# Kernel optimization log

Hardware: AMD Instinct MI355X
Metric: run time of the kernel (lower is better)

## Reference

```python
import jax, jax.numpy as jnp
import numpy as np

N_QUBITS = 8   # out_channels = number of wires
KERNEL = 4     # kernel_size
N_LAYERS = 4
STRIDE = 1
PAD = 1


def _rx(t):
    c = jnp.cos(t * 0.5).astype(jnp.complex64)
    s = jnp.sin(t * 0.5).astype(jnp.complex64)
    return jnp.stack([jnp.stack([c, -1j * s]), jnp.stack([-1j * s, c])])


def _ry(t):
    c = jnp.cos(t * 0.5).astype(jnp.complex64)
    s = jnp.sin(t * 0.5).astype(jnp.complex64)
    return jnp.stack([jnp.stack([c, -s]), jnp.stack([s, c])])


def _rz(t):
    e = jnp.exp(-0.5j * t.astype(jnp.complex64))
    z = jnp.zeros((), jnp.complex64)
    return jnp.stack([jnp.stack([e, z]), jnp.stack([z, jnp.conj(e)])])


def _ap1(state, U, w):
    # apply 2x2 gate U on qubit axis w of state shaped (2,)*N_QUBITS
    s = jnp.moveaxis(state, w, -1)
    s = s @ U.T
    return jnp.moveaxis(s, -1, w)


def _cnot(state, c, t):
    s0 = jax.lax.index_in_dim(state, 0, axis=c, keepdims=True)
    s1 = jax.lax.index_in_dim(state, 1, axis=c, keepdims=True)
    return jnp.concatenate([s0, jnp.flip(s1, axis=t)], axis=c)


def _ansatz(state, wl):  # wl: (N_QUBITS, 3) angles for layer i (custom_layers)
    for j in range(N_QUBITS):
        c, t = (j, j + 1) if j < N_QUBITS - 1 else (0, j)
        state = _ap1(state, _rx(wl[j, 0]), j)
        state = _cnot(state, c, t)
        state = _ap1(state, _ry(wl[j, 1]), j)
        state = _cnot(state, c, t)
        state = _ap1(state, _rz(wl[j, 2]), j)
    return state


def _circuit(inputs, weights):
    # inputs: (KERNEL,) patch; weights: (N_LAYERS+1, N_QUBITS, 3)
    state = jnp.zeros((2,) * N_QUBITS, jnp.complex64).at[(0,) * N_QUBITS].set(1.0)
    state = _ansatz(state, weights[0])
    for i in range(1, N_LAYERS + 1):
        w = 0
        for _ in range(N_QUBITS // KERNEL):  # 'parallel': re-upload data each layer
            for k in range(KERNEL):
                state = _ap1(state, _ry(inputs[k]), w + k)
            w += KERNEL
        state = _ansatz(state, weights[i])
    probs = state.real ** 2 + state.imag ** 2
    sign = jnp.array([1.0, -1.0], jnp.float32)
    z = [jnp.sum(probs, axis=tuple(a for a in range(N_QUBITS) if a != j)) @ sign
         for j in range(N_QUBITS)]
    return jnp.stack(z)  # (N_QUBITS,) <PauliZ_j>


def _forward(vector, weights):
    bs, ch, l = vector.shape
    if ch > 1:
        vector = vector.mean(axis=-2).reshape(bs, 1, l)
    v = jnp.pad(vector, ((0, 0), (0, 0), (PAD, PAD)))
    l_out = (l + 2 * PAD - KERNEL) // STRIDE + 1
    idx = jnp.arange(l_out)[:, None] * STRIDE + jnp.arange(KERNEL)  # (l_out, K)
    patches = v[:, 0, :][:, idx].reshape(bs * l_out, KERNEL)
    q = jax.vmap(_circuit, in_axes=(0, None))(patches, weights)  # (bs*l_out, N_QUBITS)
    out = q.reshape(bs, l_out, N_QUBITS).transpose(0, 2, 1)  # (bs, C, l_out)
    out = jax.nn.relu(out)
    return jnp.max(out, axis=-1, keepdims=True)  # (bs, C, 1)


def setup_inputs() -> dict:
    key = jax.random.key(0)
    k1, k2 = jax.random.split(key)
    vector = jax.random.normal(k1, (8, 1, 512), jnp.float32)
    # flax nn.initializers.normal() default stddev = 0.01
    weights = jax.random.normal(k2, (N_LAYERS + 1, N_QUBITS, 3), jnp.float32) * 0.01
    return {"vector": vector, "weights": weights}


def reference(vector, weights):
    return _forward(vector, weights)
```

## Files before the change

### kernel.cpp

```cpp
#include <hip/hip_runtime.h>

#define NQ 8
#define KK 4
#define LIN 512
#define LOUT 511
#define BATCH 8
#define NCIRC (BATCH * LOUT)

__device__ float g_tab[240];
__device__ float g_st0[512];

template<int M> __device__ __forceinline__ float lx(float v) {
    if constexpr (M == 1)
        return __builtin_bit_cast(float, __builtin_amdgcn_update_dpp(
            0, __builtin_bit_cast(int, v), 0xB1, 0xF, 0xF, true));
    else if constexpr (M == 2)
        return __builtin_bit_cast(float, __builtin_amdgcn_update_dpp(
            0, __builtin_bit_cast(int, v), 0x4E, 0xF, 0xF, true));
    else if constexpr (M == 3)
        return __builtin_bit_cast(float, __builtin_amdgcn_update_dpp(
            0, __builtin_bit_cast(int, v), 0x1B, 0xF, 0xF, true));
    else if constexpr (M == 8)
        return __builtin_bit_cast(float, __builtin_amdgcn_update_dpp(
            0, __builtin_bit_cast(int, v), 0x128, 0xF, 0xF, true));
    else if constexpr (M < 32)
        return __builtin_bit_cast(float, __builtin_amdgcn_ds_swizzle(
            __builtin_bit_cast(int, v), (M << 10) | 0x1F));
    else
        return __shfl_xor(v, M, 64);
}

template<int BP>
__device__ __forceinline__ void g_rx4(float (&sr)[4], float (&si)[4], float c, float s, int lane) {
    if constexpr (BP >= 2) {
        constexpr int M = 1 << (BP - 2);
        #pragma unroll
        for (int r = 0; r < 4; ++r) {
            float orr = lx<M>(sr[r]), oii = lx<M>(si[r]);
            float nr = c * sr[r] + s * oii;
            float ni = c * si[r] - s * orr;
            sr[r] = nr; si[r] = ni;
        }
    } else if constexpr (BP == 1) {
        #pragma unroll
        for (int p = 0; p < 2; ++p) {
            const int a = p, b = p + 2;
            float ar = sr[a], ai = si[a], br = sr[b], bi = si[b];
            sr[a] = c*ar + s*bi;  si[a] = c*ai - s*br;
            sr[b] = c*br + s*ai;  si[b] = c*bi - s*ar;
        }
    } else {
        #pragma unroll
        for (int p = 0; p < 2; ++p) {
            const int a = 2*p, b = 2*p + 1;
            float ar = sr[a], ai = si[a], br = sr[b], bi = si[b];
            sr[a] = c*ar + s*bi;  si[a] = c*ai - s*br;
            sr[b] = c*br + s*ai;  si[b] = c*bi - s*ar;
        }
    }
}

template<int BP>
__device__ __forceinline__ void g_rz4(float (&sr)[4], float (&si)[4], float c, float s, int lane) {
    if constexpr (BP >= 2) {
        const float t = ((lane >> (BP - 2)) & 1) ? -s : s;
        #pragma unroll
        for (int r = 0; r < 4; ++r) {
            float nr = c * sr[r] + t * si[r];
            float ni = c * si[r] - t * sr[r];
            sr[r] = nr; si[r] = ni;
        }
    } else if constexpr (BP == 1) {
        #pragma unroll
        for (int r = 0; r < 4; ++r) {
            const float t = (r < 2) ? s : -s;
            float nr = c * sr[r] + t * si[r];
            float ni = c * si[r] - t * sr[r];
            sr[r] = nr; si[r] = ni;
        }
    } else {
        #pragma unroll
        for (int r = 0; r < 4; ++r) {
            const float t = ((r & 1) == 0) ? s : -s;
            float nr = c * sr[r] + t * si[r];
            float ni = c * si[r] - t * sr[r];
            sr[r] = nr; si[r] = ni;
        }
    }
}

template<int BPC, int BPT>
__device__ __forceinline__ void g_fry4(float (&sr)[4], float (&si)[4], float c, float s, int lane) {
    if constexpr (BPT >= 2) {
        constexpr int M = (1 << (BPC - 2)) | (1 << (BPT - 2));
        const float sg = ((lane >> (BPC - 2)) & 1) ? s : -s;
        #pragma unroll
        for (int r = 0; r < 4; ++r) {
            float orr = lx<M>(sr[r]), oii = lx<M>(si[r]);
            sr[r] = c * sr[r] + sg * orr;
            si[r] = c * si[r] + sg * oii;
        }
    } else if constexpr (BPT == 1) {
        constexpr int M = 1 << (BPC - 2);
        const float sg = ((lane >> (BPC - 2)) & 1) ? s : -s;
        float pr[4], pi[4];
        #pragma unroll
        for (int r = 0; r < 4; ++r) { pr[r] = lx<M>(sr[r ^ 2]); pi[r] = lx<M>(si[r ^ 2]); }
        #pragma unroll
        for (int r = 0; r < 4; ++r) { sr[r] = c*sr[r] + sg*pr[r]; si[r] = c*si[r] + sg*pi[r]; }
    } else if constexpr (BPC == 1) {
        float t0r = sr[0], t0i = si[0], t1r = sr[1], t1i = si[1];
        sr[0] = c*sr[0] - s*sr[3];  si[0] = c*si[0] - s*si[3];
        sr[1] = c*sr[1] - s*sr[2];  si[1] = c*si[1] - s*si[2];
        sr[2] = c*sr[2] + s*t1r;    si[2] = c*si[2] + s*t1i;
        sr[3] = c*sr[3] + s*t0r;    si[3] = c*si[3] + s*t0i;
    } else {
        constexpr int M = 1 << (BPC - 2);
        const float sg = ((lane >> (BPC - 2)) & 1) ? s : -s;
        float pr[4], pi[4];
        #pragma unroll
        for (int r = 0; r < 4; ++r) { pr[r] = lx<M>(sr[r ^ 1]); pi[r] = lx<M>(si[r ^ 1]); }
        #pragma unroll
        for (int r = 0; r < 4; ++r) { sr[r] = c*sr[r] + sg*pr[r]; si[r] = c*si[r] + sg*pi[r]; }
    }
}

__device__ __forceinline__ void g_cry4_q7(float (&sr)[4], float (&si)[4], float c, float s, int lane) {
    const float se = ((lane >> 5) & 1) ? -s : s;
    #pragma unroll
    for (int p = 0; p < 2; ++p) {
        const int a = 2*p, b = 2*p + 1;
        float ar = sr[a], ai = si[a], br = sr[b], bi = si[b];
        sr[a] = c*ar - se*br;  si[a] = c*ai - se*bi;
        sr[b] = se*ar + c*br;  si[b] = se*ai + c*bi;
    }
}

template<int J>
__device__ __forceinline__ void astep4(float (&sr)[4], float (&si)[4],
                                       const float* __restrict__ t48, int lane) {
    constexpr int BP = 7 - J;
    g_rx4<BP>(sr, si, t48[J*6 + 0], t48[J*6 + 1], lane);
    if constexpr (J < 7) {
        g_fry4<7 - J, 6 - J>(sr, si, t48[J*6 + 2], t48[J*6 + 3], lane);
    } else {
        g_cry4_q7(sr, si, t48[J*6 + 2], t48[J*6 + 3], lane);
    }
    g_rz4<BP>(sr, si, t48[J*6 + 4], t48[J*6 + 5], lane);
}

template<int LB>
__device__ __forceinline__ void rx_lane(float (&sr)[8], float (&si)[8], float c, float s) {
    constexpr int M = 1 << LB;
    #pragma unroll
    for (int r = 0; r < 8; ++r) {
        float orr = lx<M>(sr[r]), oii = lx<M>(si[r]);
        float nr = c * sr[r] + s * oii;
        float ni = c * si[r] - s * orr;
        sr[r] = nr; si[r] = ni;
    }
}

template<int LB>
__device__ __forceinline__ void ry_lane(float (&sr)[8], float (&si)[8], float c, float s, int lane) {
    constexpr int M = 1 << LB;
    const float sg = ((lane >> LB) & 1) ? s : -s;
    #pragma unroll
    for (int r = 0; r < 8; ++r) {
        float orr = lx<M>(sr[r]), oii = lx<M>(si[r]);
        sr[r] = c * sr[r] + sg * orr;
        si[r] = c * si[r] + sg * oii;
    }
}

template<int LB>
__device__ __forceinline__ void rz_lane(float (&sr)[8], float (&si)[8], float c, float s, int lane) {
    const float t = ((lane >> LB) & 1) ? -s : s;
    #pragma unroll
    for (int r = 0; r < 8; ++r) {
        float nr = c * sr[r] + t * si[r];
        float ni = c * si[r] - t * sr[r];
        sr[r] = nr; si[r] = ni;
    }
}

template<int RB>
__device__ __forceinline__ void rx_reg(float (&sr)[8], float (&si)[8], float c, float s) {
    constexpr int m = 1 << RB;
    #pragma unroll
    for (int r = 0; r < 8; ++r) {
        if ((r & m) == 0) {
            const int a = r, b = r | m;
            float ar = sr[a], ai = si[a], br = sr[b], bi = si[b];
            sr[a] = c*ar + s*bi;  si[a] = c*ai - s*br;
            sr[b] = c*br + s*ai;  si[b] = c*bi - s*ar;
        }
    }
}

template<int RB>
__device__ __forceinline__ void ry_reg(float (&sr)[8], float (&si)[8], float c, float s) {
    constexpr int m = 1 << RB;
    #pragma unroll
    for (int r = 0; r < 8; ++r) {
        if ((r & m) == 0) {
            const int a = r, b = r | m;
            float ar = sr[a], ai = si[a], br = sr[b], bi = si[b];
            sr[a] = c*ar - s*br;  si[a] = c*ai - s*bi;
            sr[b] = s*ar + c*br;  si[b] = s*ai + c*bi;
        }
    }
}

template<int RB>
__device__ __forceinline__ void rz_reg(float (&sr)[8], float (&si)[8], float c, float s) {
    #pragma unroll
    for (int r = 0; r < 8; ++r) {
        const float t = ((r >> RB) & 1) ? -s : s;
        float nr = c * sr[r] + t * si[r];
        float ni = c * si[r] - t * sr[r];
        sr[r] = nr; si[r] = ni;
    }
}

template<int LBc, int LBt>
__device__ __forceinline__ void fry_ll(float (&sr)[8], float (&si)[8], float c, float s, int lane) {
    constexpr int M = (1 << LBc) | (1 << LBt);
    const float sg = ((lane >> LBc) & 1) ? s : -s;
    #pragma unroll
    for (int r = 0; r < 8; ++r) {
        float orr = lx<M>(sr[r]), oii = lx<M>(si[r]);
        sr[r] = c * sr[r] + sg * orr;
        si[r] = c * si[r] + sg * oii;
    }
}

template<int LBc, int RBt>
__device__ __forceinline__ void fry_lr(float (&sr)[8], float (&si)[8], float c, float s, int lane) {
    constexpr int M = 1 << LBc;
    constexpr int mt = 1 << RBt;
    const float sg = ((lane >> LBc) & 1) ? s : -s;
    float pr[8], pi[8];
    #pragma unroll
    for (int r = 0; r < 8; ++r) { pr[r] = lx<M>(sr[r ^ mt]); pi[r] = lx<M>(si[r ^ mt]); }
    #pragma unroll
    for (int r = 0; r < 8; ++r) { sr[r] = c*sr[r] + sg*pr[r]; si[r] = c*si[r] + sg*pi[r]; }
}

template<int RBc, int RBt>
__device__ __forceinline__ void fry_rr(float (&sr)[8], float (&si)[8], float c, float s) {
    constexpr int mm = (1 << RBc) | (1 << RBt);
    float nr[8], ni[8];
    #pragma unroll
    for (int r = 0; r < 8; ++r) {
        const float sg = ((r >> RBc) & 1) ? s : -s;
        nr[r] = c*sr[r] + sg*sr[r ^ mm];
        ni[r] = c*si[r] + sg*si[r ^ mm];
    }
    #pragma unroll
    for (int r = 0; r < 8; ++r) { sr[r] = nr[r]; si[r] = ni[r]; }
}

__device__ __forceinline__ void cry_q7(float (&sr)[8], float (&si)[8], float c, float s, int lane) {
    const float se = ((lane >> 4) & 1) ? -s : s;
    #pragma unroll
    for (int p = 0; p < 4; ++p) {
        const int a = 2*p, b = 2*p + 1;
        float ar = sr[a], ai = si[a], br = sr[b], bi = si[b];
        sr[a] = c*ar - se*br;  si[a] = c*ai - se*bi;
        sr[b] = se*ar + c*br;  si[b] = se*ai + c*bi;
    }
}

template<bool LAST>
__device__ __forceinline__ void ansatz8(float (&sr)[8], float (&si)[8],
                                        const float* __restrict__ t, int lane) {
    rx_lane<4>(sr, si, t[0], t[1]);
    fry_ll<4,3>(sr, si, t[2], t[3], lane);
    if (!LAST) rz_lane<4>(sr, si, t[4], t[5], lane);
    rx_lane<3>(sr, si, t[6], t[7]);
    fry_ll<3,2>(sr, si, t[8], t[9], lane);
    if (!LAST) rz_lane<3>(sr, si, t[10], t[11], lane);
    rx_lane<2>(sr, si, t[12], t[13]);
    fry_ll<2,1>(sr, si, t[14], t[15], lane);
    if (!LAST) rz_lane<2>(sr, si, t[16], t[17], lane);
    rx_lane<1>(sr, si, t[18], t[19]);
    fry_ll<1,0>(sr, si, t[20], t[21], lane);
    if (!LAST) rz_lane<1>(sr, si, t[22], t[23], lane);
    rx_lane<0>(sr, si, t[24], t[25]);
    fry_lr<0,2>(sr, si, t[26], t[27], lane);
    if (!LAST) rz_lane<0>(sr, si, t[28], t[29], lane);
    rx_reg<2>(sr, si, t[30], t[31]);
    fry_rr<2,1>(sr, si, t[32], t[33]);
    if (!LAST) rz_reg<2>(sr, si, t[34], t[35]);
    rx_reg<1>(sr, si, t[36], t[37]);
    fry_rr<1,0>(sr, si, t[38], t[39]);
    if (!LAST) rz_reg<1>(sr, si, t[40], t[41]);
    rx_reg<0>(sr, si, t[42], t[43]);
    cry_q7(sr, si, t[44], t[45], lane);
    if (!LAST) rz_reg<0>(sr, si, t[46], t[47]);
}

__device__ __forceinline__ void reup8(float (&sr)[8], float (&si)[8],
                                      const float (&xc)[4], const float (&xs)[4], int lane) {
    ry_lane<4>(sr, si, xc[0], xs[0], lane);  ry_lane<0>(sr, si, xc[0], xs[0], lane);
    ry_lane<3>(sr, si, xc[1], xs[1], lane);  ry_reg<2>(sr, si, xc[1], xs[1]);
    ry_lane<2>(sr, si, xc[2], xs[2], lane);  ry_reg<1>(sr, si, xc[2], xs[2]);
    ry_lane<1>(sr, si, xc[3], xs[3], lane);  ry_reg<0>(sr, si, xc[3], xs[3]);
}

template<int ST>
__device__ __forceinline__ void bstage8(float (&z)[8], int lane) {
    constexpr int M = 1 << ST;
    #pragma unroll
    for (int q = 0; q < 8; ++q) {
        float o = lx<M>(z[q]);
        if (q < 5 && (4 - q) == ST)
            z[q] = ((lane >> ST) & 1) ? (o - z[q]) : (z[q] - o);
        else
            z[q] += o;
    }
}

__global__ __launch_bounds__(256) void prep_kernel(const float* __restrict__ wts,
                                                   float* __restrict__ out) {
    __shared__ float tt[240];
    const int t = threadIdx.x;
    if (t < 120) {
        float a = 0.5f * wts[t];
        float cv = __cosf(a), sv = __sinf(a);
        g_tab[2*t] = cv;  g_tab[2*t + 1] = sv;
        tt[2*t] = cv;     tt[2*t + 1] = sv;
    }
    if (t >= 192 && t < 192 + BATCH * NQ) out[t - 192] = 0.0f;
    __syncthreads();
    if (t < 64) {
        const int lane = t;
        float sr[4] = {0.f, 0.f, 0.f, 0.f};
        float si[4] = {0.f, 0.f, 0.f, 0.f};
        if (lane == 0) sr[0] = 1.0f;
        astep4<0>(sr, si, tt, lane); astep4<1>(sr, si, tt, lane);
        astep4<2>(sr, si, tt, lane); astep4<3>(sr, si, tt, lane);
        astep4<4>(sr, si, tt, lane); astep4<5>(sr, si, tt, lane);
        astep4<6>(sr, si, tt, lane); astep4<7>(sr, si, tt, lane);
        #pragma unroll
        for (int r = 0; r < 4; ++r) {
            g_st0[(lane*4 + r)*2]     = sr[r];
            g_st0[(lane*4 + r)*2 + 1] = si[r];
        }
    }
}

__global__ __launch_bounds__(256) void quanv_kernel(const float* __restrict__ vec,
                                                    float* __restrict__ out) {
    const int tid = threadIdx.x;
    const int lane = tid & 63;
    const int pos = tid & 31;
    const int circ = blockIdx.x * 8 + (tid >> 5);
    const int b = circ / LOUT;
    const int op = circ - b * LOUT;

    float xc[4], xs[4];
    #pragma unroll
    for (int k = 0; k < KK; ++k) {
        int idx = op - 1 + k;
        int ic = idx < 0 ? 0 : (idx > LIN - 1 ? LIN - 1 : idx);
        float xv = vec[b * LIN + ic];
        xv = (idx == ic) ? xv : 0.0f;
        float a = 0.5f * xv;
        xs[k] = __sinf(a); xc[k] = __cosf(a);
    }

    float sr[8], si[8];
    {
        const float4* st4 = (const float4*)g_st0;
        #pragma unroll
        for (int h = 0; h < 4; ++h) {
            float4 v4 = st4[pos * 4 + h];
            sr[2*h]   = v4.x; si[2*h]   = v4.y;
            sr[2*h+1] = v4.z; si[2*h+1] = v4.w;
        }
    }

    #pragma unroll 1
    for (int L = 1; L <= 3; ++L) {
        reup8(sr, si, xc, xs, lane);
        ansatz8<false>(sr, si, g_tab + L * 48, lane);
    }
    reup8(sr, si, xc, xs, lane);
    ansatz8<true>(sr, si, g_tab + 4 * 48, lane);

    float p[8];
    #pragma unroll
    for (int r = 0; r < 8; ++r) p[r] = sr[r]*sr[r] + si[r]*si[r];
    float pl = 0.f, z5 = 0.f, z6 = 0.f, z7 = 0.f;
    #pragma unroll
    for (int r = 0; r < 8; ++r) {
        pl += p[r];
        z5 += ((r >> 2) & 1) ? -p[r] : p[r];
        z6 += ((r >> 1) & 1) ? -p[r] : p[r];
        z7 += ( r       & 1) ? -p[r] : p[r];
    }
    float z[8];
    z[0] = pl; z[1] = pl; z[2] = pl; z[3] = pl; z[4] = pl;
    z[5] = z5; z[6] = z6; z[7] = z7;

    bstage8<0>(z, lane); bstage8<1>(z, lane); bstage8<2>(z, lane);
    bstage8<3>(z, lane); bstage8<4>(z, lane);

    __shared__ float zsh[8][NQ];
    __shared__ int bsh[8];
    const int g = tid >> 5;
    if (pos == 0) {
        bsh[g] = b;
        #pragma unroll
        for (int q = 0; q < NQ; ++q) zsh[g][q] = fmaxf(z[q], 0.0f);
    }
    __syncthreads();
    if (tid < 64) {
        const int gg = tid >> 3, q = tid & 7;
        const bool leader = (gg == 0) || (bsh[gg] != bsh[gg - 1]);
        if (leader) {
            float m = zsh[gg][q];
            for (int g2 = gg + 1; g2 < 8 && bsh[g2] == bsh[gg]; ++g2)
                m = fmaxf(m, zsh[g2][q]);
            atomicMax((unsigned int*)(out + bsh[gg] * NQ + q), __float_as_uint(m));
        }
    }
}

extern "C" void kernel_launch(void* const* d_in, const int* in_sizes, int n_in,
                              void* d_out, int out_size, void* d_ws, size_t ws_size,
                              hipStream_t stream) {
    const float* vec = (const float*)d_in[0];
    const float* wts = (const float*)d_in[1];
    float* out = (float*)d_out;

    hipLaunchKernelGGL(prep_kernel, dim3(1), dim3(256), 0, stream, wts, out);
    const int blocks = NCIRC / 8;
    hipLaunchKernelGGL(quanv_kernel, dim3(blocks), dim3(256), 0, stream, vec, out);
}
```

Measured before the change: 75.45 us.

## Fuse prep kernel into main kernel with in-kernel trig and last-block finalize

```diff
diff --git a/kernel.cpp b/kernel.cpp
--- a/kernel.cpp
+++ b/kernel.cpp
@@ -6,9 +6,11 @@
 #define LOUT 511
 #define BATCH 8
 #define NCIRC (BATCH * LOUT)
-
-__device__ float g_tab[240];
-__device__ float g_st0[512];
+#define NBLOCKS (NCIRC / 8)
+
+#define ENC0 0xC0000000u
+__device__ unsigned g_acc[BATCH * NQ];
+__device__ unsigned g_cnt;
 
 template<int M> __device__ __forceinline__ float lx(float v) {
     if constexpr (M == 1)
@@ -23,130 +25,9 @@
     else if constexpr (M == 8)
         return __builtin_bit_cast(float, __builtin_amdgcn_update_dpp(
             0, __builtin_bit_cast(int, v), 0x128, 0xF, 0xF, true));
-    else if constexpr (M < 32)
+    else
         return __builtin_bit_cast(float, __builtin_amdgcn_ds_swizzle(
             __builtin_bit_cast(int, v), (M << 10) | 0x1F));
-    else
-        return __shfl_xor(v, M, 64);
-}
-
-template<int BP>
-__device__ __forceinline__ void g_rx4(float (&sr)[4], float (&si)[4], float c, float s, int lane) {
-    if constexpr (BP >= 2) {
-        constexpr int M = 1 << (BP - 2);
-        #pragma unroll
-        for (int r = 0; r < 4; ++r) {
-            float orr = lx<M>(sr[r]), oii = lx<M>(si[r]);
-            float nr = c * sr[r] + s * oii;
-            float ni = c * si[r] - s * orr;
-            sr[r] = nr; si[r] = ni;
-        }
-    } else if constexpr (BP == 1) {
-        #pragma unroll
-        for (int p = 0; p < 2; ++p) {
-            const int a = p, b = p + 2;
-            float ar = sr[a], ai = si[a], br = sr[b], bi = si[b];
-            sr[a] = c*ar + s*bi;  si[a] = c*ai - s*br;
-            sr[b] = c*br + s*ai;  si[b] = c*bi - s*ar;
-        }
-    } else {
-        #pragma unroll
-        for (int p = 0; p < 2; ++p) {
-            const int a = 2*p, b = 2*p + 1;
-            float ar = sr[a], ai = si[a], br = sr[b], bi = si[b];
-            sr[a] = c*ar + s*bi;  si[a] = c*ai - s*br;
-            sr[b] = c*br + s*ai;  si[b] = c*bi - s*ar;
-        }
-    }
-}
-
-template<int BP>
-__device__ __forceinline__ void g_rz4(float (&sr)[4], float (&si)[4], float c, float s, int lane) {
-    if constexpr (BP >= 2) {
-        const float t = ((lane >> (BP - 2)) & 1) ? -s : s;
-        #pragma unroll
-        for (int r = 0; r < 4; ++r) {
-            float nr = c * sr[r] + t * si[r];
-            float ni = c * si[r] - t * sr[r];
-            sr[r] = nr; si[r] = ni;
-        }
-    } else if constexpr (BP == 1) {
-        #pragma unroll
-        for (int r = 0; r < 4; ++r) {
-            const float t = (r < 2) ? s : -s;
-            float nr = c * sr[r] + t * si[r];
-            float ni = c * si[r] - t * sr[r];
-            sr[r] = nr; si[r] = ni;
-        }
-    } else {
-        #pragma unroll
-        for (int r = 0; r < 4; ++r) {
-            const float t = ((r & 1) == 0) ? s : -s;
-            float nr = c * sr[r] + t * si[r];
-            float ni = c * si[r] - t * sr[r];
-            sr[r] = nr; si[r] = ni;
-        }
-    }
-}
-
-template<int BPC, int BPT>
-__device__ __forceinline__ void g_fry4(float (&sr)[4], float (&si)[4], float c, float s, int lane) {
-    if constexpr (BPT >= 2) {
-        constexpr int M = (1 << (BPC - 2)) | (1 << (BPT - 2));
-        const float sg = ((lane >> (BPC - 2)) & 1) ? s : -s;
-        #pragma unroll
-        for (int r = 0; r < 4; ++r) {
-            float orr = lx<M>(sr[r]), oii = lx<M>(si[r]);
-            sr[r] = c * sr[r] + sg * orr;
-            si[r] = c * si[r] + sg * oii;
-        }
-    } else if constexpr (BPT == 1) {
-        constexpr int M = 1 << (BPC - 2);
-        const float sg = ((lane >> (BPC - 2)) & 1) ? s : -s;
-        float pr[4], pi[4];
-        #pragma unroll
-        for (int r = 0; r < 4; ++r) { pr[r] = lx<M>(sr[r ^ 2]); pi[r] = lx<M>(si[r ^ 2]); }
-        #pragma unroll
-        for (int r = 0; r < 4; ++r) { sr[r] = c*sr[r] + sg*pr[r]; si[r] = c*si[r] + sg*pi[r]; }
-    } else if constexpr (BPC == 1) {
-        float t0r = sr[0], t0i = si[0], t1r = sr[1], t1i = si[1];
-        sr[0] = c*sr[0] - s*sr[3];  si[0] = c*si[0] - s*si[3];
-        sr[1] = c*sr[1] - s*sr[2];  si[1] = c*si[1] - s*si[2];
-        sr[2] = c*sr[2] + s*t1r;    si[2] = c*si[2] + s*t1i;
-        sr[3] = c*sr[3] + s*t0r;    si[3] = c*si[3] + s*t0i;
-    } else {
-        constexpr int M = 1 << (BPC - 2);
-        const float sg = ((lane >> (BPC - 2)) & 1) ? s : -s;
-        float pr[4], pi[4];
-        #pragma unroll
-        for (int r = 0; r < 4; ++r) { pr[r] = lx<M>(sr[r ^ 1]); pi[r] = lx<M>(si[r ^ 1]); }
-        #pragma unroll
-        for (int r = 0; r < 4; ++r) { sr[r] = c*sr[r] + sg*pr[r]; si[r] = c*si[r] + sg*pi[r]; }
-    }
-}
-
-__device__ __forceinline__ void g_cry4_q7(float (&sr)[4], float (&si)[4], float c, float s, int lane) {
-    const float se = ((lane >> 5) & 1) ? -s : s;
-    #pragma unroll
-    for (int p = 0; p < 2; ++p) {
-        const int a = 2*p, b = 2*p + 1;
-        float ar = sr[a], ai = si[a], br = sr[b], bi = si[b];
-        sr[a] = c*ar - se*br;  si[a] = c*ai - se*bi;
-        sr[b] = se*ar + c*br;  si[b] = se*ai + c*bi;
-    }
-}
-
-template<int J>
-__device__ __forceinline__ void astep4(float (&sr)[4], float (&si)[4],
-                                       const float* __restrict__ t48, int lane) {
-    constexpr int BP = 7 - J;
-    g_rx4<BP>(sr, si, t48[J*6 + 0], t48[J*6 + 1], lane);
-    if constexpr (J < 7) {
-        g_fry4<7 - J, 6 - J>(sr, si, t48[J*6 + 2], t48[J*6 + 3], lane);
-    } else {
-        g_cry4_q7(sr, si, t48[J*6 + 2], t48[J*6 + 3], lane);
-    }
-    g_rz4<BP>(sr, si, t48[J*6 + 4], t48[J*6 + 5], lane);
 }
 
 template<int LB>
@@ -274,31 +155,31 @@
 
 template<bool LAST>
 __device__ __forceinline__ void ansatz8(float (&sr)[8], float (&si)[8],
-                                        const float* __restrict__ t, int lane) {
-    rx_lane<4>(sr, si, t[0], t[1]);
-    fry_ll<4,3>(sr, si, t[2], t[3], lane);
-    if (!LAST) rz_lane<4>(sr, si, t[4], t[5], lane);
-    rx_lane<3>(sr, si, t[6], t[7]);
-    fry_ll<3,2>(sr, si, t[8], t[9], lane);
-    if (!LAST) rz_lane<3>(sr, si, t[10], t[11], lane);
-    rx_lane<2>(sr, si, t[12], t[13]);
-    fry_ll<2,1>(sr, si, t[14], t[15], lane);
-    if (!LAST) rz_lane<2>(sr, si, t[16], t[17], lane);
-    rx_lane<1>(sr, si, t[18], t[19]);
-    fry_ll<1,0>(sr, si, t[20], t[21], lane);
-    if (!LAST) rz_lane<1>(sr, si, t[22], t[23], lane);
-    rx_lane<0>(sr, si, t[24], t[25]);
-    fry_lr<0,2>(sr, si, t[26], t[27], lane);
-    if (!LAST) rz_lane<0>(sr, si, t[28], t[29], lane);
-    rx_reg<2>(sr, si, t[30], t[31]);
-    fry_rr<2,1>(sr, si, t[32], t[33]);
-    if (!LAST) rz_reg<2>(sr, si, t[34], t[35]);
-    rx_reg<1>(sr, si, t[36], t[37]);
-    fry_rr<1,0>(sr, si, t[38], t[39]);
-    if (!LAST) rz_reg<1>(sr, si, t[40], t[41]);
-    rx_reg<0>(sr, si, t[42], t[43]);
-    cry_q7(sr, si, t[44], t[45], lane);
-    if (!LAST) rz_reg<0>(sr, si, t[46], t[47]);
+                                        const float (&tc)[24], const float (&ts)[24], int lane) {
+    rx_lane<4>(sr, si, tc[0], ts[0]);
+    fry_ll<4,3>(sr, si, tc[1], ts[1], lane);
+    if (!LAST) rz_lane<4>(sr, si, tc[2], ts[2], lane);
+    rx_lane<3>(sr, si, tc[3], ts[3]);
+    fry_ll<3,2>(sr, si, tc[4], ts[4], lane);
+    if (!LAST) rz_lane<3>(sr, si, tc[5], ts[5], lane);
+    rx_lane<2>(sr, si, tc[6], ts[6]);
+    fry_ll<2,1>(sr, si, tc[7], ts[7], lane);
+    if (!LAST) rz_lane<2>(sr, si, tc[8], ts[8], lane);
+    rx_lane<1>(sr, si, tc[9], ts[9]);
+    fry_ll<1,0>(sr, si, tc[10], ts[10], lane);
+    if (!LAST) rz_lane<1>(sr, si, tc[11], ts[11], lane);
+    rx_lane<0>(sr, si, tc[12], ts[12]);
+    fry_lr<0,2>(sr, si, tc[13], ts[13], lane);
+    if (!LAST) rz_lane<0>(sr, si, tc[14], ts[14], lane);
+    rx_reg<2>(sr, si, tc[15], ts[15]);
+    fry_rr<2,1>(sr, si, tc[16], ts[16]);
+    if (!LAST) rz_reg<2>(sr, si, tc[17], ts[17]);
+    rx_reg<1>(sr, si, tc[18], ts[18]);
+    fry_rr<1,0>(sr, si, tc[19], ts[19]);
+    if (!LAST) rz_reg<1>(sr, si, tc[20], ts[20]);
+    rx_reg<0>(sr, si, tc[21], ts[21]);
+    cry_q7(sr, si, tc[22], ts[22], lane);
+    if (!LAST) rz_reg<0>(sr, si, tc[23], ts[23]);
 }
 
 __device__ __forceinline__ void reup8(float (&sr)[8], float (&si)[8],
@@ -322,36 +203,22 @@
     }
 }
 
-__global__ __launch_bounds__(256) void prep_kernel(const float* __restrict__ wts,
-                                                   float* __restrict__ out) {
-    __shared__ float tt[240];
-    const int t = threadIdx.x;
-    if (t < 120) {
-        float a = 0.5f * wts[t];
-        float cv = __cosf(a), sv = __sinf(a);
-        g_tab[2*t] = cv;  g_tab[2*t + 1] = sv;
-        tt[2*t] = cv;     tt[2*t + 1] = sv;
-    }
-    if (t >= 192 && t < 192 + BATCH * NQ) out[t - 192] = 0.0f;
-    __syncthreads();
-    if (t < 64) {
-        const int lane = t;
-        float sr[4] = {0.f, 0.f, 0.f, 0.f};
-        float si[4] = {0.f, 0.f, 0.f, 0.f};
-        if (lane == 0) sr[0] = 1.0f;
-        astep4<0>(sr, si, tt, lane); astep4<1>(sr, si, tt, lane);
-        astep4<2>(sr, si, tt, lane); astep4<3>(sr, si, tt, lane);
-        astep4<4>(sr, si, tt, lane); astep4<5>(sr, si, tt, lane);
-        astep4<6>(sr, si, tt, lane); astep4<7>(sr, si, tt, lane);
-        #pragma unroll
-        for (int r = 0; r < 4; ++r) {
-            g_st0[(lane*4 + r)*2]     = sr[r];
-            g_st0[(lane*4 + r)*2 + 1] = si[r];
-        }
+__device__ __forceinline__ void layer_trig(const float* __restrict__ wl,
+                                           float (&tc)[24], float (&ts)[24], int lane) {
+    float a = (lane < 24) ? 0.5f * wl[lane] : 0.0f;
+    float s, c;
+    __sincosf(a, &s, &c);
+    #pragma unroll
+    for (int i = 0; i < 24; ++i) {
+        tc[i] = __builtin_bit_cast(float,
+            __builtin_amdgcn_readlane(__builtin_bit_cast(int, c), i));
+        ts[i] = __builtin_bit_cast(float,
+            __builtin_amdgcn_readlane(__builtin_bit_cast(int, s), i));
     }
 }
 
 __global__ __launch_bounds__(256) void quanv_kernel(const float* __restrict__ vec,
+                                                    const float* __restrict__ wts,
                                                     float* __restrict__ out) {
     const int tid = threadIdx.x;
     const int lane = tid & 63;
@@ -371,24 +238,23 @@
         xs[k] = __sinf(a); xc[k] = __cosf(a);
     }
 
-    float sr[8], si[8];
-    {
-        const float4* st4 = (const float4*)g_st0;
-        #pragma unroll
-        for (int h = 0; h < 4; ++h) {
-            float4 v4 = st4[pos * 4 + h];
-            sr[2*h]   = v4.x; si[2*h]   = v4.y;
-            sr[2*h+1] = v4.z; si[2*h+1] = v4.w;
-        }
-    }
+    float sr[8] = {0,0,0,0,0,0,0,0};
+    float si[8] = {0,0,0,0,0,0,0,0};
+    if (pos == 0) sr[0] = 1.0f;
+
+    float tc[24], ts[24];
+    layer_trig(wts, tc, ts, lane);
+    ansatz8<false>(sr, si, tc, ts, lane);
 
     #pragma unroll 1
     for (int L = 1; L <= 3; ++L) {
+        layer_trig(wts + L * 24, tc, ts, lane);
         reup8(sr, si, xc, xs, lane);
-        ansatz8<false>(sr, si, g_tab + L * 48, lane);
-    }
+        ansatz8<false>(sr, si, tc, ts, lane);
+    }
+    layer_trig(wts + 4 * 24, tc, ts, lane);
     reup8(sr, si, xc, xs, lane);
-    ansatz8<true>(sr, si, g_tab + 4 * 48, lane);
+    ansatz8<true>(sr, si, tc, ts, lane);
 
     float p[8];
     #pragma unroll
@@ -410,6 +276,7 @@
 
     __shared__ float zsh[8][NQ];
     __shared__ int bsh[8];
+    __shared__ int lastFlag;
     const int g = tid >> 5;
     if (pos == 0) {
         bsh[g] = b;
@@ -424,8 +291,22 @@
             float m = zsh[gg][q];
             for (int g2 = gg + 1; g2 < 8 && bsh[g2] == bsh[gg]; ++g2)
                 m = fmaxf(m, zsh[g2][q]);
-            atomicMax((unsigned int*)(out + bsh[gg] * NQ + q), __float_as_uint(m));
+            atomicMax(&g_acc[bsh[gg] * NQ + q], __float_as_uint(m) + ENC0);
         }
+    }
+    __syncthreads();
+
+    if (tid == 0) {
+        __threadfence();
+        unsigned old = atomicAdd(&g_cnt, 1u);
+        lastFlag = (old == NBLOCKS - 1);
+    }
+    __syncthreads();
+    if (lastFlag && tid < BATCH * NQ) {
+        unsigned e = atomicMax(&g_acc[tid], 0u);
+        out[tid] = __uint_as_float(e - ENC0);
+        g_acc[tid] = ENC0;
+        if (tid == 0) g_cnt = 0u;
     }
 }
 
@@ -436,7 +317,5 @@
     const float* wts = (const float*)d_in[1];
     float* out = (float*)d_out;
 
-    hipLaunchKernelGGL(prep_kernel, dim3(1), dim3(256), 0, stream, wts, out);
-    const int blocks = NCIRC / 8;
-    hipLaunchKernelGGL(quanv_kernel, dim3(blocks), dim3(256), 0, stream, vec, out);
-}
+    hipLaunchKernelGGL(quanv_kernel, dim3(NBLOCKS), dim3(256), 0, stream, vec, wts, out);
+}
```

New measurement: 77.59 us. 1.03x slower.
